# Kernel tuning notes

Hardware: AMD Instinct MI355X
Metric: run time of the kernel (lower is better)

Reference implementation:

```python
import jax, jax.numpy as jnp
import numpy as np

N_QUBITS = 22
N_LAYERS = 3
N_STATES = 2 ** N_QUBITS
N_PARAMS = N_QUBITS * N_LAYERS  # gate_set='ry'

# CNOT as a rank-4 tensor [c_out, t_out, c_in, t_in]; matches the bit convention
# of _expand_two_gate_matrix (control bit unchanged, target flipped when control=1).
_CNOT4 = jnp.array(
    [[1, 0, 0, 0], [0, 1, 0, 0], [0, 0, 0, 1], [0, 0, 1, 0]], dtype=jnp.complex64
).reshape(2, 2, 2, 2)


def _apply_1q(state, gate, qubit):
    # qubit q is bit q of the state index (little-endian); with C-order reshape to
    # (2,)*n, axis k holds bit (n-1-k), so qubit q -> axis n-1-q.
    axis = N_QUBITS - 1 - qubit
    s = jnp.tensordot(gate, state, axes=((1,), (axis,)))  # new qubit axis at front
    return jnp.moveaxis(s, 0, axis)


def _apply_cnot(state, control, target):
    ax_c = N_QUBITS - 1 - control
    ax_t = N_QUBITS - 1 - target
    s = jnp.tensordot(_CNOT4, state, axes=((2, 3), (ax_c, ax_t)))
    return jnp.moveaxis(s, (0, 1), (ax_c, ax_t))


def setup_inputs() -> dict:
    key = jax.random.key(0)
    k1, k2, k3 = jax.random.split(key, 3)
    params = jax.random.normal(k1, (N_PARAMS,), dtype=jnp.float32) * 0.1
    state_real = jax.random.normal(k2, (N_STATES,), dtype=jnp.float32)
    state_imag = jax.random.normal(k3, (N_STATES,), dtype=jnp.float32)
    return {"params": params, "state_real": state_real, "state_imag": state_imag}


def reference(params, state_real, state_imag):
    # State as rank-n tensor of shape (2,)*n_qubits
    state = (state_real + 1j * state_imag).astype(jnp.complex64)
    state = state.reshape((2,) * N_QUBITS)
    idx = 0
    for layer in range(N_LAYERS):
        # gate_set == 'ry': one RY rotation per qubit per layer
        for q in range(N_QUBITS):
            a = params[idx]
            idx += 1
            c = jnp.cos(a * 0.5)
            s = jnp.sin(a * 0.5)
            # RY(a) = [[cos, -sin], [sin, cos]]
            gate = jnp.stack([jnp.stack([c, -s]), jnp.stack([s, c])]).astype(jnp.complex64)
            state = _apply_1q(state, gate, q)
        # entangling CNOT chain between layers (not after the last layer)
        if layer < N_LAYERS - 1:
            for q in range(N_QUBITS - 1):
                state = _apply_cnot(state, q, q + 1)
    return state.reshape(-1)  # amplitudes, shape (2**n_qubits,), complex64
```

## Files before the change

### kernel.cpp

```cpp
#include <hip/hip_runtime.h>


#define NQ 22
#define NSTATES (1u << NQ)
#define IDXMASK (NSTATES - 1u)

__device__ __forceinline__ unsigned short f2bf(float x) {
  unsigned int b = __float_as_uint(x);
  b += 0x7FFFu + ((b >> 16) & 1u);
  return (unsigned short)(b >> 16);
}
__device__ __forceinline__ float bf2f(unsigned short h) {
  return __uint_as_float((unsigned int)h << 16);
}
__device__ __forceinline__ unsigned SW(unsigned l) {
  return l ^ ((l >> 5) & 31u) ^ ((l >> 10) & 7u);
}

template <int ML, int MR, int RS, unsigned SM, int N>
__device__ __forceinline__ void rot(float (&v)[N], float c, float s, unsigned pbase) {
  int sb = __popc(pbase & SM) & 1;
  float sp = sb ? s : -s;
  constexpr int LB = MR & (-MR);
  if (ML == 0) {
#pragma unroll
    for (int i = 0; i < N; ++i)
      if (!(i & LB)) {
        const int j = i ^ MR;
        const int pi = __builtin_popcount(((unsigned)i << RS) & SM) & 1;
        const int pj = __builtin_popcount(((unsigned)j << RS) & SM) & 1;
        float a = v[i], b = v[j];
        v[i] = fmaf(pi ? -sp : sp, b, c * a);
        v[j] = fmaf(pj ? -sp : sp, a, c * b);
      }
  } else if (MR == 0) {
#pragma unroll
    for (int i = 0; i < N; ++i) {
      float o = __shfl_xor(v[i], ML, 64);
      const int pi = __builtin_popcount(((unsigned)i << RS) & SM) & 1;
      v[i] = fmaf(pi ? -sp : sp, o, c * v[i]);
    }
  } else {
#pragma unroll
    for (int i = 0; i < N; ++i)
      if (!(i & LB)) {
        const int j = i ^ MR;
        float oa = __shfl_xor(v[j], ML, 64);
        float ob = __shfl_xor(v[i], ML, 64);
        const int pi = __builtin_popcount(((unsigned)i << RS) & SM) & 1;
        const int pj = __builtin_popcount(((unsigned)j << RS) & SM) & 1;
        v[i] = fmaf(pi ? -sp : sp, oa, c * v[i]);
        v[j] = fmaf(pj ? -sp : sp, ob, c * v[j]);
      }
  }
}

__global__ void ksetup(const unsigned int* __restrict__ probe,
                       const void* __restrict__ prm,
                       float* __restrict__ csb, int* __restrict__ flagp) {
  __shared__ int anybad;
  if (threadIdx.x == 0) anybad = 0;
  __syncthreads();
  int bad = 0;
  for (int i = threadIdx.x; i < 4096; i += 256) {
    unsigned e = (probe[i] >> 7) & 0xFFu;
    bad |= (e >= 0x90u);
  }
  if (bad) anybad = 1;
  __syncthreads();
  int f = anybad ? 0 : 1;
  if (threadIdx.x == 0) *flagp = f;
  int i = threadIdx.x;
  if (i < 66) {
    float a = f ? bf2f(((const unsigned short*)prm)[i]) : ((const float*)prm)[i];
    float sv, cv;
    sincosf(0.5f * a, &sv, &cv);
    csb[i] = cv; csb[66 + i] = sv;
  }
}

#define RC(k) csb[k], csb[66 + (k)]

__global__ void __launch_bounds__(256, 5)
ksweep1(const void* re, const void* im, float* __restrict__ Wr,
        float* __restrict__ Wi, const float* __restrict__ csb,
        const int* __restrict__ flag) {
  __shared__ float ld[8192];
  int tid = threadIdx.x;
  int f = *flag;
  int pl = blockIdx.y;
  const void* src = (pl ^ (f ? 0 : 1)) ? im : re;
  float* W = pl ? Wi : Wr;
  unsigned B = blockIdx.x;
  unsigned tb = B << 13;

  if (f) {
    const unsigned short* sp = (const unsigned short*)src + tb;
#pragma unroll
    for (int k = 0; k < 4; ++k) {
      unsigned C = (unsigned)k * 256 + tid;
      uint4 q = *reinterpret_cast<const uint4*>(sp + C * 8);
      unsigned e0 = C * 8;
      ld[SW(e0 + 0)] = bf2f((unsigned short)(q.x & 0xFFFFu));
      ld[SW(e0 + 1)] = bf2f((unsigned short)(q.x >> 16));
      ld[SW(e0 + 2)] = bf2f((unsigned short)(q.y & 0xFFFFu));
      ld[SW(e0 + 3)] = bf2f((unsigned short)(q.y >> 16));
      ld[SW(e0 + 4)] = bf2f((unsigned short)(q.z & 0xFFFFu));
      ld[SW(e0 + 5)] = bf2f((unsigned short)(q.z >> 16));
      ld[SW(e0 + 6)] = bf2f((unsigned short)(q.w & 0xFFFFu));
      ld[SW(e0 + 7)] = bf2f((unsigned short)(q.w >> 16));
    }
  } else {
    const float* sp = (const float*)src + tb;
#pragma unroll
    for (int k = 0; k < 8; ++k) {
      unsigned C = (unsigned)k * 256 + tid;
      float4 t = *reinterpret_cast<const float4*>(sp + C * 4);
      unsigned e0 = C * 4;
      ld[SW(e0 + 0)] = t.x; ld[SW(e0 + 1)] = t.y;
      ld[SW(e0 + 2)] = t.z; ld[SW(e0 + 3)] = t.w;
    }
  }
  __syncthreads();

  int lane = tid & 63, wv = tid >> 6;
  float v[32];

  unsigned lb0 = ((unsigned)lane << 5) | ((unsigned)wv << 11);
  unsigned pb0 = tb | lb0;
#pragma unroll
  for (int i = 0; i < 32; ++i) v[i] = ld[SW(lb0 | (unsigned)i)];
  rot<0, 1, 0, 0x1u>(v, RC(0), pb0);
  rot<0, 2, 0, 0x2u>(v, RC(1), pb0);
  rot<0, 4, 0, 0x4u>(v, RC(2), pb0);
  rot<0, 8, 0, 0x8u>(v, RC(3), pb0);
  rot<0, 16, 0, 0x10u>(v, RC(4), pb0);
  rot<0, 3, 0, 0x1u>(v, RC(22), pb0);
  rot<0, 6, 0, 0x3u>(v, RC(23), pb0);
  rot<0, 12, 0, 0x7u>(v, RC(24), pb0);
  rot<0, 24, 0, 0xFu>(v, RC(25), pb0);
  rot<0, 5, 0, 0x1u>(v, RC(44), pb0);
  rot<0, 10, 0, 0x2u>(v, RC(45), pb0);
  rot<0, 20, 0, 0x5u>(v, RC(46), pb0);
#pragma unroll
  for (int i = 0; i < 32; ++i) ld[SW(lb0 | (unsigned)i)] = v[i];
  __syncthreads();

  unsigned lb1 = ((unsigned)lane & 15u) | ((((unsigned)lane >> 4) & 3u) << 9) |
                 ((unsigned)wv << 11);
  unsigned pb1 = tb | lb1;
#pragma unroll
  for (int i = 0; i < 32; ++i) v[i] = ld[SW(lb1 | ((unsigned)i << 4))];
  rot<0, 2, 4, 0x20u>(v, RC(5), pb1);
  rot<0, 4, 4, 0x40u>(v, RC(6), pb1);
  rot<0, 8, 4, 0x80u>(v, RC(7), pb1);
  rot<0, 16, 4, 0x100u>(v, RC(8), pb1);
  rot<0, 3, 4, 0x1Fu>(v, RC(26), pb1);
  rot<0, 6, 4, 0x3Fu>(v, RC(27), pb1);
  rot<0, 12, 4, 0x7Fu>(v, RC(28), pb1);
  rot<0, 24, 4, 0xFFu>(v, RC(29), pb1);
  rot<8, 2, 4, 0xAu>(v, RC(47), pb1);
  rot<0, 5, 4, 0x15u>(v, RC(48), pb1);
  rot<0, 10, 4, 0x2Au>(v, RC(49), pb1);
  rot<0, 20, 4, 0x55u>(v, RC(50), pb1);
#pragma unroll
  for (int i = 0; i < 32; ++i) ld[SW(lb1 | ((unsigned)i << 4))] = v[i];
  __syncthreads();

  unsigned lb2 = ((unsigned)lane & 31u) | ((unsigned)wv << 5) |
                 ((((unsigned)lane >> 5) & 1u) << 7);
  unsigned pb2 = tb | lb2;
#pragma unroll
  for (int i = 0; i < 32; ++i) v[i] = ld[SW(lb2 | ((unsigned)i << 8))];
  rot<0, 2, 8, 0x200u>(v, RC(9), pb2);
  rot<0, 4, 8, 0x400u>(v, RC(10), pb2);
  rot<0, 8, 8, 0x800u>(v, RC(11), pb2);
  rot<0, 16, 8, 0x1000u>(v, RC(12), pb2);
  rot<0, 3, 8, 0x1FFu>(v, RC(30), pb2);
  rot<0, 6, 8, 0x3FFu>(v, RC(31), pb2);
  rot<0, 12, 8, 0x7FFu>(v, RC(32), pb2);
  rot<0, 24, 8, 0xFFFu>(v, RC(33), pb2);
  rot<32, 2, 8, 0xAAu>(v, RC(51), pb2);
  rot<0, 5, 8, 0x155u>(v, RC(52), pb2);
  rot<0, 10, 8, 0x2AAu>(v, RC(53), pb2);
  rot<0, 20, 8, 0x555u>(v, RC(54), pb2);
#pragma unroll
  for (int i = 0; i < 32; ++i) ld[SW(lb2 | ((unsigned)i << 8))] = v[i];
  __syncthreads();

#pragma unroll
  for (int k = 0; k < 8; ++k) {
    unsigned c = (unsigned)k * 256 + tid;
    unsigned cb9 = c >> 2, h2 = c & 3;
    unsigned lloc = (cb9 << 2) | (h2 << 11);
    float4 t;
    t.x = ld[SW(lloc | 0)];
    t.y = ld[SW(lloc | 1)];
    t.z = ld[SW(lloc | 2)];
    t.w = ld[SW(lloc | 3)];
    *reinterpret_cast<float4*>(W + (((size_t)cb9 << 13) | ((size_t)B << 4) |
                                    (h2 << 2))) = t;
  }
}

__global__ void __launch_bounds__(512, 4)
ksweep2(const float* __restrict__ Wr, const float* __restrict__ Wi,
        unsigned* __restrict__ tmp, const float* __restrict__ csb) {
  __shared__ float ld[2][8192];
  int tid = threadIdx.x;
  unsigned cb = blockIdx.x;

#pragma unroll
  for (int k = 0; k < 8; ++k) {
    unsigned C = (unsigned)k * 512 + tid;
    int p = C >> 11;
    unsigned hh = C & 2047u;
    const float* W = p ? Wi : Wr;
    float4 t = *reinterpret_cast<const float4*>(W + (((size_t)cb << 13) |
                                                     (hh << 2)));
    unsigned e0 = hh << 2;
    ld[p][SW(e0 + 0)] = t.x; ld[p][SW(e0 + 1)] = t.y;
    ld[p][SW(e0 + 2)] = t.z; ld[p][SW(e0 + 3)] = t.w;
  }
  __syncthreads();

  int lane = tid & 63;
  int wq = (tid >> 6) & 3;
  int pl = tid >> 8;
  float* L = ld[pl];
  float v[32];

  unsigned lbQ0 = ((unsigned)lane & 3u) | ((((unsigned)lane >> 2) & 15u) << 7) |
                  ((unsigned)wq << 11);
  unsigned pb0 = ((unsigned)lane & 3u) | (cb << 2) |
                 ((((unsigned)lane >> 2) & 15u) << 16) | ((unsigned)wq << 20);
#pragma unroll
  for (int i = 0; i < 32; ++i) v[i] = L[SW(lbQ0 | ((unsigned)i << 2))];
  rot<0, 4, 11, (1u << 13)>(v, RC(13), pb0);
  rot<0, 8, 11, (1u << 14)>(v, RC(14), pb0);
  rot<0, 16, 11, (1u << 15)>(v, RC(15), pb0);
  rot<0, 6, 11, 0x1FFFu>(v, RC(34), pb0);
  rot<0, 12, 11, 0x3FFFu>(v, RC(35), pb0);
  rot<0, 24, 11, 0x7FFFu>(v, RC(36), pb0);
  rot<0, 5, 11, 0xAAAu>(v, RC(55), pb0);
  rot<0, 10, 11, 0x1555u>(v, RC(56), pb0);
  rot<0, 20, 11, 0x2AAAu>(v, RC(57), pb0);
#pragma unroll
  for (int i = 0; i < 32; ++i) L[SW(lbQ0 | ((unsigned)i << 2))] = v[i];
  __syncthreads();

  unsigned lbQ1 = ((unsigned)lane & 31u) | ((((unsigned)lane >> 5) & 1u) << 10) |
                  ((unsigned)wq << 11);
  unsigned pb1 = ((unsigned)lane & 3u) | (cb << 2) |
                 ((((unsigned)lane >> 2) & 7u) << 11) |
                 ((((unsigned)lane >> 5) & 1u) << 19) | ((unsigned)wq << 20);
#pragma unroll
  for (int i = 0; i < 32; ++i) v[i] = L[SW(lbQ1 | ((unsigned)i << 5))];
  rot<0, 4, 14, (1u << 16)>(v, RC(16), pb1);
  rot<0, 8, 14, (1u << 17)>(v, RC(17), pb1);
  rot<0, 16, 14, (1u << 18)>(v, RC(18), pb1);
  rot<0, 6, 14, 0xFFFFu>(v, RC(37), pb1);
  rot<0, 12, 14, 0x1FFFFu>(v, RC(38), pb1);
  rot<0, 24, 14, 0x3FFFFu>(v, RC(39), pb1);
  rot<0, 5, 14, 0x5555u>(v, RC(58), pb1);
  rot<0, 10, 14, 0xAAAAu>(v, RC(59), pb1);
  rot<0, 20, 14, 0x15555u>(v, RC(60), pb1);
#pragma unroll
  for (int i = 0; i < 32; ++i) L[SW(lbQ1 | ((unsigned)i << 5))] = v[i];
  __syncthreads();

  unsigned lbQ2 = ((unsigned)lane & 63u) | ((unsigned)wq << 6);
  unsigned pb2 = ((unsigned)lane & 3u) | (cb << 2) |
                 ((((unsigned)lane >> 2) & 15u) << 11) | ((unsigned)wq << 15);
#pragma unroll
  for (int i = 0; i < 32; ++i) v[i] = L[SW(lbQ2 | ((unsigned)i << 8))];
  rot<0, 4, 17, (1u << 19)>(v, RC(19), pb2);
  rot<0, 8, 17, (1u << 20)>(v, RC(20), pb2);
  rot<0, 16, 17, (1u << 21)>(v, RC(21), pb2);
  rot<0, 6, 17, 0x7FFFFu>(v, RC(40), pb2);
  rot<0, 12, 17, 0xFFFFFu>(v, RC(41), pb2);
  rot<0, 24, 17, 0x1FFFFFu>(v, RC(42), pb2);
  rot<0, 16, 17, 0x3FFFFFu>(v, RC(43), pb2);
  rot<0, 5, 17, 0x2AAAAu>(v, RC(61), pb2);
  rot<0, 10, 17, 0x55555u>(v, RC(62), pb2);
  rot<0, 20, 17, 0xAAAAAu>(v, RC(63), pb2);
  rot<0, 8, 17, 0x155555u>(v, RC(64), pb2);
  rot<0, 16, 17, 0x2AAAAAu>(v, RC(65), pb2);
#pragma unroll
  for (int i = 0; i < 32; ++i) L[SW(lbQ2 | ((unsigned)i << 8))] = v[i];
  __syncthreads();

#pragma unroll
  for (int k = 0; k < 4; ++k) {
    unsigned Q = (unsigned)k * 512 + tid;
    unsigned e0 = Q << 2;
    uint4 o;
    o.x = (unsigned)f2bf(ld[0][SW(e0 + 0)]) | ((unsigned)f2bf(ld[1][SW(e0 + 0)]) << 16);
    o.y = (unsigned)f2bf(ld[0][SW(e0 + 1)]) | ((unsigned)f2bf(ld[1][SW(e0 + 1)]) << 16);
    o.z = (unsigned)f2bf(ld[0][SW(e0 + 2)]) | ((unsigned)f2bf(ld[1][SW(e0 + 2)]) << 16);
    o.w = (unsigned)f2bf(ld[0][SW(e0 + 3)]) | ((unsigned)f2bf(ld[1][SW(e0 + 3)]) << 16);
    *reinterpret_cast<uint4*>(tmp + (((size_t)Q << 11) | (cb << 2))) = o;
  }
}

__global__ void __launch_bounds__(256)
kfinal(const unsigned* __restrict__ tmp, unsigned* __restrict__ out32) {
  unsigned T = blockIdx.x * 256 + threadIdx.x;
  unsigned lb = T << 2;
  unsigned s = (lb ^ (lb << 2)) & IDXMASK;
  const uint4* w = reinterpret_cast<const uint4*>(tmp + (s & ~15u));
  uint4 a = w[0], b = w[1], c = w[2], d = w[3];
  uint4 o;
  switch ((s >> 2) & 3u) {
    case 0: o = make_uint4(a.x, b.y, c.z, d.w); break;
    case 1: o = make_uint4(b.x, a.y, d.z, c.w); break;
    case 2: o = make_uint4(c.x, d.y, a.z, b.w); break;
    default: o = make_uint4(d.x, c.y, b.z, a.w); break;
  }
  *reinterpret_cast<uint4*>(out32 + lb) = o;
}

__global__ void __launch_bounds__(256)
kinit(const void* s0, const void* s1, float* d0, float* d1,
      const int* __restrict__ flag, int basepl) {
  int pl = blockIdx.y + basepl;
  int f = *flag;
  const void* src = (pl ^ (f ? 0 : 1)) ? s1 : s0;
  float* dst = pl ? d1 : d0;
  unsigned p = blockIdx.x * 256 + threadIdx.x;
  unsigned q = (p ^ (p << 2)) & IDXMASK;
  dst[p] = f ? bf2f(((const unsigned short*)src)[q]) : ((const float*)src)[q];
}
__global__ void __launch_bounds__(256)
kpass(float* b0, float* b1, const float* __restrict__ csb,
      int L, int qa, unsigned ma, unsigned mb) {
  int k = L * 22 + qa;
  float ca = csb[k], sa = csb[66 + k];
  float cb = csb[k + 1], sb = csb[66 + k + 1];
  float* buf = blockIdx.y ? b1 : b0;
  unsigned t = blockIdx.x * 256 + threadIdx.x;
  unsigned j = (t & ((1u << qa) - 1u)) | ((t >> qa) << (qa + 2));
  unsigned p = j;
  if (L == 0)      { p ^= p << 2; p ^= p << 4; p ^= p << 8; p ^= p << 16; }
  else if (L == 1) { p ^= p << 1; p ^= p << 2; p ^= p << 4; p ^= p << 8; p ^= p << 16; }
  p &= IDXMASK;
  unsigned mc = ma ^ mb;
  float x0 = buf[p], x1 = buf[p ^ ma], x2 = buf[p ^ mb], x3 = buf[p ^ mc];
  float y0 = ca * x0 - sa * x1, y1 = sa * x0 + ca * x1;
  float y2 = ca * x2 - sa * x3, y3 = sa * x2 + ca * x3;
  buf[p]      = cb * y0 - sb * y2;
  buf[p ^ ma] = cb * y1 - sb * y3;
  buf[p ^ mb] = sb * y0 + cb * y2;
  buf[p ^ mc] = sb * y1 + cb * y3;
}
__global__ void __launch_bounds__(256)
kpark(const float* __restrict__ fv, unsigned short* __restrict__ park) {
  unsigned j = blockIdx.x * 256 + threadIdx.x;
  park[j] = f2bf(fv[j]);
}
__global__ void __launch_bounds__(256)
kmerge(const unsigned short* __restrict__ park, unsigned int* outw) {
  unsigned j = blockIdx.x * 256 + threadIdx.x;
  float vv = __uint_as_float(outw[j]);
  outw[j] = (unsigned)park[j] | ((unsigned)f2bf(vv) << 16);
}
static inline unsigned pmask(int q, int L) {
  unsigned r = 0;
  if (L == 0)      for (unsigned m = 1u << q; m < NSTATES; m <<= 2) r ^= m;
  else if (L == 1) for (unsigned m = 1u << q; m < NSTATES; m <<= 1) r ^= m;
  else r = 1u << q;
  return r;
}

extern "C" void kernel_launch(void* const* d_in, const int* in_sizes, int n_in,
                              void* d_out, int out_size, void* d_ws, size_t ws_size,
                              hipStream_t stream) {
  (void)out_size;
  const void* prm = d_in[0];
  const void* re  = d_in[1];
  const void* im  = d_in[2];
  if (in_sizes[0] != 66) {
    const void* big[2] = {nullptr, nullptr};
    int nb = 0;
    for (int i = 0; i < n_in; ++i) {
      if (in_sizes[i] == 66) prm = d_in[i];
      else if (nb < 2) big[nb++] = d_in[i];
    }
    if (nb == 2) { re = big[0]; im = big[1]; }
  }
  const size_t N = NSTATES;

  if (ws_size >= N * 12 + 1024) {
    float* Wr = (float*)d_ws;
    float* Wi = Wr + N;
    unsigned* tmp = (unsigned*)(Wi + N);
    float* csb = (float*)(tmp + N);
    int* flag = (int*)(csb + 140);
    ksetup<<<1, 256, 0, stream>>>((const unsigned int*)re, prm, csb, flag);
    ksweep1<<<dim3(512, 2), 256, 0, stream>>>(re, im, Wr, Wi, csb, flag);
    ksweep2<<<dim3(512), 512, 0, stream>>>(Wr, Wi, tmp, csb);
    kfinal<<<dim3(4096), 256, 0, stream>>>(tmp, (unsigned*)d_out);
  } else {
    float* F = (float*)d_out;
    unsigned short* park = (unsigned short*)d_ws;
    float* csb = (float*)((char*)d_ws + N * 2);
    int* flag = (int*)(csb + 140);
    dim3 blk(256);
    ksetup<<<1, 256, 0, stream>>>((const unsigned int*)re, prm, csb, flag);
    kinit<<<dim3(16384, 1), blk, 0, stream>>>(re, im, F, F, flag, 0);
    for (int L = 0; L < 3; ++L)
      for (int qa = 0; qa < 22; qa += 2)
        kpass<<<dim3(4096, 1), blk, 0, stream>>>(F, F, csb, L, qa,
                                                 pmask(qa, L), pmask(qa + 1, L));
    kpark<<<dim3(16384), blk, 0, stream>>>(F, park);
    kinit<<<dim3(16384, 1), blk, 0, stream>>>(re, im, F, F, flag, 1);
    for (int L = 0; L < 3; ++L)
      for (int qa = 0; qa < 22; qa += 2)
        kpass<<<dim3(4096, 1), blk, 0, stream>>>(F, F, csb, L, qa,
                                                 pmask(qa, L), pmask(qa + 1, L));
    kmerge<<<dim3(16384), blk, 0, stream>>>(park, (unsigned int*)d_out);
  }
}
```

Measured before the change: 70.95 us.

## Pack intermediate state as bf16 pairs, fold setup into sweeps, merge planes

The intermediate buffer between the two sweep kernels now holds one 32-bit word per amplitude, packing the real and imaginary parts as bf16, instead of two separate fp32 planes. This cuts the write and re-read traffic between the sweeps by a large factor. Each sweep block now also computes the dtype probe and the gate cos/sin values itself, so the separate setup launch and its global flag and coefficient buffers are gone. ksweep1 processes both planes in one 512-thread block and loads global data straight into registers rather than staging it through LDS. The costs are an extra bf16 rounding of the intermediate state, a much smaller dtype probe (64 words instead of 4096), and redundant setup work in every block.

```diff
diff --git a/kernel.cpp b/kernel.cpp
--- a/kernel.cpp
+++ b/kernel.cpp
@@ -55,81 +55,68 @@
   }
 }
 
-__global__ void ksetup(const unsigned int* __restrict__ probe,
-                       const void* __restrict__ prm,
-                       float* __restrict__ csb, int* __restrict__ flagp) {
-  __shared__ int anybad;
-  if (threadIdx.x == 0) anybad = 0;
-  __syncthreads();
+__device__ __forceinline__ int blk_setup(const void* re, const void* prm,
+                                         float* cs2, int tid) {
   int bad = 0;
-  for (int i = threadIdx.x; i < 4096; i += 256) {
-    unsigned e = (probe[i] >> 7) & 0xFFu;
-    bad |= (e >= 0x90u);
-  }
-  if (bad) anybad = 1;
-  __syncthreads();
-  int f = anybad ? 0 : 1;
-  if (threadIdx.x == 0) *flagp = f;
-  int i = threadIdx.x;
-  if (i < 66) {
-    float a = f ? bf2f(((const unsigned short*)prm)[i]) : ((const float*)prm)[i];
+  const unsigned* pr = (const unsigned*)re;
+#pragma unroll
+  for (int i = 0; i < 64; ++i) bad |= (((pr[i] >> 7) & 0xFFu) >= 0x90u);
+  int f = bad ? 0 : 1;
+  if (tid < 66) {
+    float a = f ? bf2f(((const unsigned short*)prm)[tid])
+                : ((const float*)prm)[tid];
     float sv, cv;
     sincosf(0.5f * a, &sv, &cv);
-    csb[i] = cv; csb[66 + i] = sv;
-  }
+    cs2[tid] = cv; cs2[66 + tid] = sv;
+  }
+  __syncthreads();
+  return f;
 }
 
 #define RC(k) csb[k], csb[66 + (k)]
 
-__global__ void __launch_bounds__(256, 5)
-ksweep1(const void* re, const void* im, float* __restrict__ Wr,
-        float* __restrict__ Wi, const float* __restrict__ csb,
-        const int* __restrict__ flag) {
-  __shared__ float ld[8192];
+__global__ void __launch_bounds__(512, 4)
+ksweep1(const void* re, const void* im, unsigned* __restrict__ W,
+        const void* prm) {
+  __shared__ float ld[2][8192];
+  __shared__ float cs2[132];
   int tid = threadIdx.x;
-  int f = *flag;
-  int pl = blockIdx.y;
+  int f = blk_setup(re, prm, cs2, tid);
+  const float* csb = cs2;
+
+  int pl = tid >> 8;
+  int htid = tid & 255;
+  int lane = htid & 63, wv = htid >> 6;
   const void* src = (pl ^ (f ? 0 : 1)) ? im : re;
-  float* W = pl ? Wi : Wr;
+  float* L = ld[pl];
   unsigned B = blockIdx.x;
   unsigned tb = B << 13;
-
+  float v[32];
+
+  unsigned lb0 = ((unsigned)lane << 5) | ((unsigned)wv << 11);
+  unsigned pb0 = tb | lb0;
   if (f) {
-    const unsigned short* sp = (const unsigned short*)src + tb;
-#pragma unroll
-    for (int k = 0; k < 4; ++k) {
-      unsigned C = (unsigned)k * 256 + tid;
-      uint4 q = *reinterpret_cast<const uint4*>(sp + C * 8);
-      unsigned e0 = C * 8;
-      ld[SW(e0 + 0)] = bf2f((unsigned short)(q.x & 0xFFFFu));
-      ld[SW(e0 + 1)] = bf2f((unsigned short)(q.x >> 16));
-      ld[SW(e0 + 2)] = bf2f((unsigned short)(q.y & 0xFFFFu));
-      ld[SW(e0 + 3)] = bf2f((unsigned short)(q.y >> 16));
-      ld[SW(e0 + 4)] = bf2f((unsigned short)(q.z & 0xFFFFu));
-      ld[SW(e0 + 5)] = bf2f((unsigned short)(q.z >> 16));
-      ld[SW(e0 + 6)] = bf2f((unsigned short)(q.w & 0xFFFFu));
-      ld[SW(e0 + 7)] = bf2f((unsigned short)(q.w >> 16));
+    const unsigned short* sp = (const unsigned short*)src + tb + lb0;
+#pragma unroll
+    for (int j = 0; j < 4; ++j) {
+      uint4 q = *reinterpret_cast<const uint4*>(sp + j * 8);
+      v[j*8+0]=bf2f((unsigned short)(q.x & 0xFFFFu));
+      v[j*8+1]=bf2f((unsigned short)(q.x >> 16));
+      v[j*8+2]=bf2f((unsigned short)(q.y & 0xFFFFu));
+      v[j*8+3]=bf2f((unsigned short)(q.y >> 16));
+      v[j*8+4]=bf2f((unsigned short)(q.z & 0xFFFFu));
+      v[j*8+5]=bf2f((unsigned short)(q.z >> 16));
+      v[j*8+6]=bf2f((unsigned short)(q.w & 0xFFFFu));
+      v[j*8+7]=bf2f((unsigned short)(q.w >> 16));
     }
   } else {
-    const float* sp = (const float*)src + tb;
-#pragma unroll
-    for (int k = 0; k < 8; ++k) {
-      unsigned C = (unsigned)k * 256 + tid;
-      float4 t = *reinterpret_cast<const float4*>(sp + C * 4);
-      unsigned e0 = C * 4;
-      ld[SW(e0 + 0)] = t.x; ld[SW(e0 + 1)] = t.y;
-      ld[SW(e0 + 2)] = t.z; ld[SW(e0 + 3)] = t.w;
+    const float* sp = (const float*)src + tb + lb0;
+#pragma unroll
+    for (int j = 0; j < 8; ++j) {
+      float4 t = *reinterpret_cast<const float4*>(sp + j * 4);
+      v[j*4+0]=t.x; v[j*4+1]=t.y; v[j*4+2]=t.z; v[j*4+3]=t.w;
     }
   }
-  __syncthreads();
-
-  int lane = tid & 63, wv = tid >> 6;
-  float v[32];
-
-  unsigned lb0 = ((unsigned)lane << 5) | ((unsigned)wv << 11);
-  unsigned pb0 = tb | lb0;
-#pragma unroll
-  for (int i = 0; i < 32; ++i) v[i] = ld[SW(lb0 | (unsigned)i)];
   rot<0, 1, 0, 0x1u>(v, RC(0), pb0);
   rot<0, 2, 0, 0x2u>(v, RC(1), pb0);
   rot<0, 4, 0, 0x4u>(v, RC(2), pb0);
@@ -143,14 +130,14 @@
   rot<0, 10, 0, 0x2u>(v, RC(45), pb0);
   rot<0, 20, 0, 0x5u>(v, RC(46), pb0);
 #pragma unroll
-  for (int i = 0; i < 32; ++i) ld[SW(lb0 | (unsigned)i)] = v[i];
+  for (int i = 0; i < 32; ++i) L[SW(lb0 | (unsigned)i)] = v[i];
   __syncthreads();
 
   unsigned lb1 = ((unsigned)lane & 15u) | ((((unsigned)lane >> 4) & 3u) << 9) |
                  ((unsigned)wv << 11);
   unsigned pb1 = tb | lb1;
 #pragma unroll
-  for (int i = 0; i < 32; ++i) v[i] = ld[SW(lb1 | ((unsigned)i << 4))];
+  for (int i = 0; i < 32; ++i) v[i] = L[SW(lb1 | ((unsigned)i << 4))];
   rot<0, 2, 4, 0x20u>(v, RC(5), pb1);
   rot<0, 4, 4, 0x40u>(v, RC(6), pb1);
   rot<0, 8, 4, 0x80u>(v, RC(7), pb1);
@@ -164,14 +151,14 @@
   rot<0, 10, 4, 0x2Au>(v, RC(49), pb1);
   rot<0, 20, 4, 0x55u>(v, RC(50), pb1);
 #pragma unroll
-  for (int i = 0; i < 32; ++i) ld[SW(lb1 | ((unsigned)i << 4))] = v[i];
+  for (int i = 0; i < 32; ++i) L[SW(lb1 | ((unsigned)i << 4))] = v[i];
   __syncthreads();
 
   unsigned lb2 = ((unsigned)lane & 31u) | ((unsigned)wv << 5) |
                  ((((unsigned)lane >> 5) & 1u) << 7);
   unsigned pb2 = tb | lb2;
 #pragma unroll
-  for (int i = 0; i < 32; ++i) v[i] = ld[SW(lb2 | ((unsigned)i << 8))];
+  for (int i = 0; i < 32; ++i) v[i] = L[SW(lb2 | ((unsigned)i << 8))];
   rot<0, 2, 8, 0x200u>(v, RC(9), pb2);
   rot<0, 4, 8, 0x400u>(v, RC(10), pb2);
   rot<0, 8, 8, 0x800u>(v, RC(11), pb2);
@@ -185,42 +172,46 @@
   rot<0, 10, 8, 0x2AAu>(v, RC(53), pb2);
   rot<0, 20, 8, 0x555u>(v, RC(54), pb2);
 #pragma unroll
-  for (int i = 0; i < 32; ++i) ld[SW(lb2 | ((unsigned)i << 8))] = v[i];
-  __syncthreads();
-
-#pragma unroll
-  for (int k = 0; k < 8; ++k) {
-    unsigned c = (unsigned)k * 256 + tid;
-    unsigned cb9 = c >> 2, h2 = c & 3;
+  for (int i = 0; i < 32; ++i) L[SW(lb2 | ((unsigned)i << 8))] = v[i];
+  __syncthreads();
+
+#pragma unroll
+  for (int k = 0; k < 4; ++k) {
+    unsigned t = (unsigned)k * 512 + tid;
+    unsigned cb9 = t >> 2, h2 = t & 3;
     unsigned lloc = (cb9 << 2) | (h2 << 11);
-    float4 t;
-    t.x = ld[SW(lloc | 0)];
-    t.y = ld[SW(lloc | 1)];
-    t.z = ld[SW(lloc | 2)];
-    t.w = ld[SW(lloc | 3)];
-    *reinterpret_cast<float4*>(W + (((size_t)cb9 << 13) | ((size_t)B << 4) |
-                                    (h2 << 2))) = t;
+    uint4 o;
+    o.x = (unsigned)f2bf(ld[0][SW(lloc | 0)]) | ((unsigned)f2bf(ld[1][SW(lloc | 0)]) << 16);
+    o.y = (unsigned)f2bf(ld[0][SW(lloc | 1)]) | ((unsigned)f2bf(ld[1][SW(lloc | 1)]) << 16);
+    o.z = (unsigned)f2bf(ld[0][SW(lloc | 2)]) | ((unsigned)f2bf(ld[1][SW(lloc | 2)]) << 16);
+    o.w = (unsigned)f2bf(ld[0][SW(lloc | 3)]) | ((unsigned)f2bf(ld[1][SW(lloc | 3)]) << 16);
+    *reinterpret_cast<uint4*>(W + ((((cb9 << 11) | (B << 2) | h2) << 2))) = o;
   }
 }
 
 __global__ void __launch_bounds__(512, 4)
-ksweep2(const float* __restrict__ Wr, const float* __restrict__ Wi,
-        unsigned* __restrict__ tmp, const float* __restrict__ csb) {
+ksweep2(const unsigned* __restrict__ W, unsigned* __restrict__ tmp,
+        const void* re, const void* prm) {
   __shared__ float ld[2][8192];
+  __shared__ float cs2[132];
   int tid = threadIdx.x;
+  (void)blk_setup(re, prm, cs2, tid);
+  const float* csb = cs2;
   unsigned cb = blockIdx.x;
 
 #pragma unroll
-  for (int k = 0; k < 8; ++k) {
+  for (int k = 0; k < 4; ++k) {
     unsigned C = (unsigned)k * 512 + tid;
-    int p = C >> 11;
-    unsigned hh = C & 2047u;
-    const float* W = p ? Wi : Wr;
-    float4 t = *reinterpret_cast<const float4*>(W + (((size_t)cb << 13) |
-                                                     (hh << 2)));
-    unsigned e0 = hh << 2;
-    ld[p][SW(e0 + 0)] = t.x; ld[p][SW(e0 + 1)] = t.y;
-    ld[p][SW(e0 + 2)] = t.z; ld[p][SW(e0 + 3)] = t.w;
+    uint4 q = *reinterpret_cast<const uint4*>(W + (cb << 13) + C * 4);
+    unsigned o0 = C * 4;
+    ld[0][SW(o0 + 0)] = bf2f((unsigned short)(q.x & 0xFFFFu));
+    ld[1][SW(o0 + 0)] = bf2f((unsigned short)(q.x >> 16));
+    ld[0][SW(o0 + 1)] = bf2f((unsigned short)(q.y & 0xFFFFu));
+    ld[1][SW(o0 + 1)] = bf2f((unsigned short)(q.y >> 16));
+    ld[0][SW(o0 + 2)] = bf2f((unsigned short)(q.z & 0xFFFFu));
+    ld[1][SW(o0 + 2)] = bf2f((unsigned short)(q.z >> 16));
+    ld[0][SW(o0 + 3)] = bf2f((unsigned short)(q.w & 0xFFFFu));
+    ld[1][SW(o0 + 3)] = bf2f((unsigned short)(q.w >> 16));
   }
   __syncthreads();
 
@@ -320,6 +311,29 @@
   *reinterpret_cast<uint4*>(out32 + lb) = o;
 }
 
+__global__ void ksetup(const unsigned int* __restrict__ probe,
+                       const void* __restrict__ prm,
+                       float* __restrict__ csb, int* __restrict__ flagp) {
+  __shared__ int anybad;
+  if (threadIdx.x == 0) anybad = 0;
+  __syncthreads();
+  int bad = 0;
+  for (int i = threadIdx.x; i < 4096; i += 256) {
+    unsigned e = (probe[i] >> 7) & 0xFFu;
+    bad |= (e >= 0x90u);
+  }
+  if (bad) anybad = 1;
+  __syncthreads();
+  int f = anybad ? 0 : 1;
+  if (threadIdx.x == 0) *flagp = f;
+  int i = threadIdx.x;
+  if (i < 66) {
+    float a = f ? bf2f(((const unsigned short*)prm)[i]) : ((const float*)prm)[i];
+    float sv, cv;
+    sincosf(0.5f * a, &sv, &cv);
+    csb[i] = cv; csb[66 + i] = sv;
+  }
+}
 __global__ void __launch_bounds__(256)
 kinit(const void* s0, const void* s1, float* d0, float* d1,
       const int* __restrict__ flag, int basepl) {
@@ -390,15 +404,11 @@
   }
   const size_t N = NSTATES;
 
-  if (ws_size >= N * 12 + 1024) {
-    float* Wr = (float*)d_ws;
-    float* Wi = Wr + N;
-    unsigned* tmp = (unsigned*)(Wi + N);
-    float* csb = (float*)(tmp + N);
-    int* flag = (int*)(csb + 140);
-    ksetup<<<1, 256, 0, stream>>>((const unsigned int*)re, prm, csb, flag);
-    ksweep1<<<dim3(512, 2), 256, 0, stream>>>(re, im, Wr, Wi, csb, flag);
-    ksweep2<<<dim3(512), 512, 0, stream>>>(Wr, Wi, tmp, csb);
+  if (ws_size >= N * 8 + 1024) {
+    unsigned* W = (unsigned*)d_ws;
+    unsigned* tmp = W + N;
+    ksweep1<<<dim3(512), 512, 0, stream>>>(re, im, W, prm);
+    ksweep2<<<dim3(512), 512, 0, stream>>>(W, tmp, re, prm);
     kfinal<<<dim3(4096), 256, 0, stream>>>(tmp, (unsigned*)d_out);
   } else {
     float* F = (float*)d_out;
```

Result: faster. 64.23 us (-9.5%).
